# Performance work log

Measured on AMD Instinct MI355X. Metric: run time of the kernel, lower is better.

## Reference

```python
import jax, jax.numpy as jnp
import numpy as np

P_EPS = 1e-6            # nn.PairwiseDistance default eps
ALPHA = 0.25
STD_TARGET = 1.0
NUM_COMMUNITIES = 512   # C = number of unique community ids
BIG = 1e30              # masking value for hard-negative min


def setup_inputs() -> dict:
    key = jax.random.key(0)
    k1, k2, k3 = jax.random.split(key, 3)
    B, N, D, C = 1, 100000, 128, NUM_COMMUNITIES
    node_features = jax.random.normal(k1, (B, N, D), dtype=jnp.float32)
    # row 0: a permutation of node indices; row 1: community of that node.
    perm = jax.random.permutation(k2, N).astype(jnp.int32)
    comm_per_node = jnp.concatenate([
        jnp.arange(C, dtype=jnp.int32),  # guarantee every community appears
        jax.random.randint(k3, (N - C,), 0, C, dtype=jnp.int32),
    ])
    community_belong_list = jnp.stack([perm, comm_per_node[perm]])  # [2, N]
    return {"node_features": node_features, "community_belong_list": community_belong_list}


def reference(node_features, community_belong_list):
    B, N, D = node_features.shape
    C = NUM_COMMUNITIES
    dt = node_features.dtype

    # ---- _community_inverse_permute: invert row-0 permutation, reorder columns ----
    perm = community_belong_list[0]
    inv = jnp.zeros((N,), perm.dtype).at[perm].add(jnp.arange(N, dtype=perm.dtype))
    cbl = community_belong_list[:, inv]          # row0 == arange(N) after this
    comm = cbl[1]                                # [N] community id per node
    src = node_features[:, cbl[0], :]            # [B,N,D] gather (identity order)

    # ---- groupby sum / count -> community means ----
    comm_sum = jnp.zeros((B, C, D), dt).at[:, comm, :].add(src)        # [B,C,D]
    counts = jnp.zeros((C,), dt).at[comm].add(jnp.asarray(1.0, dt))   # [C]
    comm_mean = comm_sum / counts[None, :, None]                      # [B,C,D]

    # ---- cdist(node_features, comm_mean, p=2) -> [B,N,C] ----
    x2 = jnp.sum(node_features * node_features, -1)                   # [B,N]
    c2 = jnp.sum(comm_mean * comm_mean, -1)                           # [B,C]
    dots = jnp.einsum('bnd,bcd->bnc', node_features, comm_mean)
    distance = jnp.sqrt(jnp.maximum(x2[:, :, None] + c2[:, None, :] - 2.0 * dots, 0.0))

    # ---- leave-one-out community mean per node, positive distance ----
    cnt_pn = counts[comm]                                             # [N]
    cnt_m1 = jnp.maximum(cnt_pn - 1.0, 1.0)                           # [N]
    x_minus = jnp.where((cnt_pn == 1.0)[None, :, None], jnp.asarray(0.0, dt), src)
    loo_mean = (comm_sum[:, comm, :] - x_minus) / cnt_m1[None, :, None]
    pos_dist = jnp.sqrt(jnp.sum((loo_mean - src + P_EPS) ** 2, -1))   # [B,N]

    # ---- negatives: all communities except the node's own ----
    own = distance[:, jnp.arange(N), comm]                            # [B,N]
    mean_neg = (jnp.sum(distance, -1) - own) / (C - 1)                # [B,N]
    pos_mask = jnp.zeros((N, C), bool).at[jnp.arange(N), comm].set(True)
    hard_neg = jnp.min(jnp.where(pos_mask[None], jnp.asarray(BIG, dt), distance), -1)

    trip_mean = jnp.maximum(pos_dist - mean_neg + ALPHA, 0.0)
    trip_min = jnp.maximum(pos_dist - hard_neg + ALPHA, 0.0)

    # ---- groupby std (unbiased) per community per feature ----
    sq = jnp.zeros((B, C, D), dt).at[:, comm, :].add((src - comm_mean[:, comm, :]) ** 2)
    std = jnp.sqrt(sq / jnp.maximum(counts - 1.0, 1.0)[None, :, None])

    return (trip_mean.mean(), trip_min.mean(), ((std - STD_TARGET) ** 2).mean())
```

## Files before the change

### kernel.cpp

```cpp
#include <hip/hip_runtime.h>

#define NCOMM 512
#define DIM   128
#define ALPHA 0.25f
#define PEPS  1e-6f
#define BIGF  1e30f
#define TILE_C 16
#define NT    (NCOMM / TILE_C)

typedef __attribute__((ext_vector_type(8))) _Float16 f16x8;
typedef __attribute__((ext_vector_type(4))) float f32x4;

#define GLOAD_LDS16(g, l) __builtin_amdgcn_global_load_lds( \
    (const __attribute__((address_space(1))) void*)(g), \
    (__attribute__((address_space(3))) void*)(l), 16, 0, 0)


__global__ void k_inv(const int* __restrict__ cbl, int* __restrict__ inv, int N) {
    int i = blockIdx.x * 256 + threadIdx.x;
    if (i < N) inv[cbl[i]] = i;
}

__global__ void k_comm(const int* __restrict__ cbl, const int* __restrict__ inv,
                       int* __restrict__ comm, int* __restrict__ idx0,
                       int* __restrict__ counts, int N) {
    __shared__ int h[NCOMM];
    int t = threadIdx.x;
    h[t] = 0; h[t + 256] = 0;
    __syncthreads();
    int j = blockIdx.x * 256 + t;
    if (j < N) {
        int ij = inv[j];
        int c  = cbl[N + ij];
        comm[j] = c;
        idx0[j] = cbl[ij];
        atomicAdd(&h[c], 1);
    }
    __syncthreads();
    int v = h[t];        if (v) atomicAdd(&counts[t], v);
    v = h[t + 256];      if (v) atomicAdd(&counts[t + 256], v);
}

__global__ void k_scan(const int* __restrict__ counts, int* __restrict__ offsets,
                       int* __restrict__ cursor, float* __restrict__ countf) {
    __shared__ int sc[NCOMM];
    int t = threadIdx.x;
    int v0 = counts[t];
    sc[t] = v0;
    __syncthreads();
    for (int off = 1; off < NCOMM; off <<= 1) {
        int v = (t >= off) ? sc[t - off] : 0;
        __syncthreads();
        sc[t] += v;
        __syncthreads();
    }
    int excl = sc[t] - v0;
    offsets[t] = excl;
    cursor[t]  = excl;
    countf[t]  = (float)v0;
}

__global__ void k_sort(const int* __restrict__ comm, int* __restrict__ cursor,
                       int* __restrict__ sorted, int N) {
    __shared__ int h[NCOMM], hb[NCOMM];
    int t = threadIdx.x;
    h[t] = 0; h[t + 256] = 0;
    __syncthreads();
    int j0 = blockIdx.x * 1024 + t;
    int cs[4];
    #pragma unroll
    for (int q = 0; q < 4; ++q) {
        int j = j0 + q * 256;
        cs[q] = (j < N) ? comm[j] : -1;
        if (cs[q] >= 0) atomicAdd(&h[cs[q]], 1);
    }
    __syncthreads();
    int v = h[t];        if (v) hb[t] = atomicAdd(&cursor[t], v);
    v = h[t + 256];      if (v) hb[t + 256] = atomicAdd(&cursor[t + 256], v);
    __syncthreads();
    #pragma unroll
    for (int q = 0; q < 4; ++q) {
        int j = j0 + q * 256;
        if (cs[q] >= 0) {
            int p = atomicAdd(&hb[cs[q]], 1);
            sorted[p] = j;
        }
    }
}


__global__ void __launch_bounds__(256) k_stats(
        const float* __restrict__ NF, const int* __restrict__ idx0,
        const int* __restrict__ sorted, const int* __restrict__ offsets,
        const int* __restrict__ counts,
        float* __restrict__ comm_sum,
        _Float16* __restrict__ CMh, _Float16* __restrict__ CMl,
        float* __restrict__ c2, float* __restrict__ accum) {
    __shared__ int ridx[512];
    __shared__ float4 bufS[256], bufQ[256];
    int c = blockIdx.x, t = threadIdx.x;
    int d4 = t & 31, r = t >> 5;
    int cnt = counts[c], base = offsets[c];
    const float4* NF4 = (const float4*)NF;

    float4 s4 = make_float4(0.f, 0.f, 0.f, 0.f);
    float4 q4 = make_float4(0.f, 0.f, 0.f, 0.f);
    for (int chunk = 0; chunk < cnt; chunk += 512) {
        int m = min(cnt - chunk, 512);
        for (int i = t; i < m; i += 256) ridx[i] = idx0[sorted[base + chunk + i]];
        __syncthreads();
        for (int i = r; i < m; i += 8) {
            float4 v = NF4[(size_t)ridx[i] * 32 + d4];
            s4.x += v.x; s4.y += v.y; s4.z += v.z; s4.w += v.w;
            q4.x = fmaf(v.x, v.x, q4.x); q4.y = fmaf(v.y, v.y, q4.y);
            q4.z = fmaf(v.z, v.z, q4.z); q4.w = fmaf(v.w, v.w, q4.w);
        }
        __syncthreads();
    }
    bufS[t] = s4; bufQ[t] = q4;
    __syncthreads();
    if (t < 128) {
        float4 a = bufS[t], b = bufS[t + 128];
        a.x += b.x; a.y += b.y; a.z += b.z; a.w += b.w; bufS[t] = a;
        float4 e = bufQ[t], f = bufQ[t + 128];
        e.x += f.x; e.y += f.y; e.z += f.z; e.w += f.w; bufQ[t] = e;
    }
    __syncthreads();
    if (t < 64) {
        float4 a = bufS[t], b = bufS[t + 64];
        a.x += b.x; a.y += b.y; a.z += b.z; a.w += b.w; bufS[t] = a;
        float4 e = bufQ[t], f = bufQ[t + 64];
        e.x += f.x; e.y += f.y; e.z += f.z; e.w += f.w; bufQ[t] = e;
    }
    __syncthreads();
    if (t < 32) {
        float4 a = bufS[t], b = bufS[t + 32];
        a.x += b.x; a.y += b.y; a.z += b.z; a.w += b.w;
        float4 e = bufQ[t], f = bufQ[t + 32];
        e.x += f.x; e.y += f.y; e.z += f.z; e.w += f.w;
        float sarr[4] = {a.x, a.y, a.z, a.w};
        float qarr[4] = {e.x, e.y, e.z, e.w};
        float cf = (float)cnt;
        float mm = 0.f, ee = 0.f;
        #pragma unroll
        for (int k = 0; k < 4; ++k) {
            int d = t * 4 + k;
            float s = sarr[k];
            comm_sum[c * DIM + d] = s;
            float m = (cnt > 0) ? s / cf : 0.f;
            _Float16 mh = (_Float16)m;
            CMh[c * DIM + d] = mh;
            CMl[c * DIM + d] = (_Float16)(m - (float)mh);
            float varn = fmaxf(fmaf(-cf * m, m, qarr[k]), 0.f);
            float stdv = sqrtf(varn / fmaxf(cf - 1.f, 1.f));
            float er = stdv - 1.f;
            mm = fmaf(m, m, mm);
            ee = fmaf(er, er, ee);
        }
        #pragma unroll
        for (int msk = 1; msk < 32; msk <<= 1) {
            mm += __shfl_xor(mm, msk);
            ee += __shfl_xor(ee, msk);
        }
        if (t == 0) {
            c2[c] = mm;
            atomicAdd(&accum[2], ee);
        }
    }
}


__global__ void __launch_bounds__(256, 2) k_main(
        const float* __restrict__ NF,
        const _Float16* __restrict__ CMh,
        const _Float16* __restrict__ CMl,
        const float* __restrict__ comm_sum,
        const float* __restrict__ c2g,
        const float* __restrict__ countf,
        const int* __restrict__ comm,
        const int* __restrict__ idx0,
        float* __restrict__ accum, int N) {
    __shared__ _Float16 Bst[4][2][2][TILE_C * DIM];
    __shared__ float c2s[NCOMM];
    __shared__ int   comms[256];
    __shared__ float x2s[256];
    __shared__ float sums[256], mins[256];
    __shared__ float red[8];

    int tid = threadIdx.x;
    int w  = tid >> 6;
    int l  = tid & 63;
    int lr = l & 15;
    int lk = l >> 4;
    int n0 = blockIdx.x * 256;

    int goff[4];
    #pragma unroll
    for (int i = 0; i < 4; ++i) {
        int p = i * 64 + l;
        int row = p >> 4, cp = p & 15;
        goff[i] = (row * 16 + (cp ^ row)) * 8;
    }
    auto stage = [&](int tt, int b) {
        int base = tt * (TILE_C * DIM);
        _Float16* lh = &Bst[w][b][0][0];
        _Float16* ll = &Bst[w][b][1][0];
        #pragma unroll
        for (int i = 0; i < 4; ++i) {
            GLOAD_LDS16(CMh + base + goff[i], lh + i * 512);
            GLOAD_LDS16(CMl + base + goff[i], ll + i * 512);
        }
    };
    stage(0, 0);

    c2s[tid]       = c2g[tid];
    c2s[tid + 256] = c2g[tid + 256];
    {
        int gn = n0 + tid;
        comms[tid] = (gn < N) ? comm[gn] : -1;
    }

    f16x8 ah[4][4];
    #pragma unroll
    for (int mf = 0; mf < 4; ++mf) {
        int n = n0 + w * 64 + mf * 16 + lr;
        const float4* src = (const float4*)NF + (size_t)n * 32 + lk * 2;
        float p2 = 0.f;
        #pragma unroll
        for (int ks = 0; ks < 4; ++ks) {
            float4 v0 = make_float4(0.f, 0.f, 0.f, 0.f), v1 = v0;
            if (n < N) { v0 = src[ks * 8]; v1 = src[ks * 8 + 1]; }
            float fr[8] = {v0.x, v0.y, v0.z, v0.w, v1.x, v1.y, v1.z, v1.w};
            f16x8 hh;
            #pragma unroll
            for (int t = 0; t < 8; ++t) {
                hh[t] = (_Float16)fr[t];
                p2 = fmaf(fr[t], fr[t], p2);
            }
            ah[mf][ks] = hh;
        }
        p2 += __shfl_xor(p2, 16);
        p2 += __shfl_xor(p2, 32);
        if (lk == 0) x2s[w * 64 + mf * 16 + lr] = -0.5f * p2;
    }
    __syncthreads();

    int cnv[4][4];
    float sumv[4][4], minv[4][4];
    #pragma unroll
    for (int mf = 0; mf < 4; ++mf)
        #pragma unroll
        for (int j = 0; j < 4; ++j) {
            cnv[mf][j] = comms[w * 64 + mf * 16 + lk * 4 + j];
            sumv[mf][j] = 0.f; minv[mf][j] = BIGF;
        }

    int buf = 0;
    for (int tt = 0; tt < NT; ++tt) {
        if (tt + 1 < NT) {
            stage(tt + 1, buf ^ 1);
            asm volatile("s_waitcnt vmcnt(8)" ::: "memory");
        } else {
            asm volatile("s_waitcnt vmcnt(0)" ::: "memory");
        }
        __builtin_amdgcn_sched_barrier(0);

        const _Float16* bhp = &Bst[w][buf][0][0];
        const _Float16* blp = &Bst[w][buf][1][0];
        f16x8 bh[4], bl[4];
        #pragma unroll
        for (int ks = 0; ks < 4; ++ks) {
            int ch = (ks * 4 + lk) ^ lr;
            bh[ks] = *(const f16x8*)&bhp[(size_t)(lr * 16 + ch) * 8];
            bl[ks] = *(const f16x8*)&blp[(size_t)(lr * 16 + ch) * 8];
        }
        f32x4 acc[4];
        #pragma unroll
        for (int mf = 0; mf < 4; ++mf)
            acc[mf] = *(const f32x4*)&x2s[w * 64 + mf * 16 + lk * 4];

        #pragma unroll
        for (int ks = 0; ks < 4; ++ks) {
            #pragma unroll
            for (int mf = 0; mf < 4; ++mf)
                acc[mf] = __builtin_amdgcn_mfma_f32_16x16x32_f16(ah[mf][ks], bh[ks], acc[mf], 0, 0, 0);
            #pragma unroll
            for (int mf = 0; mf < 4; ++mf)
                acc[mf] = __builtin_amdgcn_mfma_f32_16x16x32_f16(ah[mf][ks], bl[ks], acc[mf], 0, 0, 0);
        }

        int ccol = tt * TILE_C + lr;
        float c2v = c2s[ccol];
        #pragma unroll
        for (int mf = 0; mf < 4; ++mf)
            #pragma unroll
            for (int j = 0; j < 4; ++j) {
                float d2 = fmaf(-2.f, acc[mf][j], c2v);
                float da = __builtin_amdgcn_sqrtf(fmaxf(d2, 0.f));
                sumv[mf][j] += da;
                minv[mf][j] = fminf(minv[mf][j], (cnv[mf][j] == ccol) ? BIGF : da);
            }
        buf ^= 1;
    }

    #pragma unroll
    for (int mf = 0; mf < 4; ++mf)
        #pragma unroll
        for (int j = 0; j < 4; ++j) {
            float sv = sumv[mf][j], mv = minv[mf][j];
            #pragma unroll
            for (int msk = 1; msk < 16; msk <<= 1) {
                sv += __shfl_xor(sv, msk);
                mv = fminf(mv, __shfl_xor(mv, msk));
            }
            if (lr == 0) {
                int idx = w * 64 + mf * 16 + lk * 4 + j;
                sums[idx] = sv; mins[idx] = mv;
            }
        }
    __syncthreads();

    float tmean = 0.f, tminv = 0.f;
    {
        int ln = tid;
        int n = n0 + ln;
        if (n < N) {
            int cnode = comms[ln];
            float cf  = countf[cnode];
            float cm1 = fmaxf(cf - 1.f, 1.f);
            float rs  = 1.f / cm1;
            bool single = (cf == 1.f);
            const float4* srow = (const float4*)(NF + (size_t)idx0[n] * DIM);
            const float4* csum = (const float4*)(comm_sum + (size_t)cnode * DIM);
            float q = 0.f, dot = 0.f;
            #pragma unroll 8
            for (int m = 0; m < 32; ++m) {
                float4 sv = srow[m];
                float4 cs = csum[m];
                float4 xm = single ? make_float4(0.f, 0.f, 0.f, 0.f) : sv;
                float lx = (cs.x - xm.x) * rs - sv.x + PEPS;
                float ly = (cs.y - xm.y) * rs - sv.y + PEPS;
                float lz = (cs.z - xm.z) * rs - sv.z + PEPS;
                float lw = (cs.w - xm.w) * rs - sv.w + PEPS;
                q = fmaf(lx, lx, fmaf(ly, ly, fmaf(lz, lz, fmaf(lw, lw, q))));
                dot = fmaf(sv.x, cs.x, fmaf(sv.y, cs.y, fmaf(sv.z, cs.z, fmaf(sv.w, cs.w, dot))));
            }
            float pos = sqrtf(q);
            float x2 = -2.f * x2s[ln];
            float ownd2 = x2 + c2s[cnode] - 2.f * (dot / cf);
            float own = sqrtf(fmaxf(ownd2, 0.f));
            float mean_neg = (sums[ln] - own) * (1.f / (float)(NCOMM - 1));
            tmean = fmaxf(pos - mean_neg + ALPHA, 0.f);
            tminv = fmaxf(pos - mins[ln] + ALPHA, 0.f);
        }
    }
    #pragma unroll
    for (int msk = 1; msk < 64; msk <<= 1) {
        tmean += __shfl_xor(tmean, msk);
        tminv += __shfl_xor(tminv, msk);
    }
    if ((tid & 63) == 0) { red[w * 2] = tmean; red[w * 2 + 1] = tminv; }
    __syncthreads();
    if (tid == 0) {
        atomicAdd(&accum[0], red[0] + red[2] + red[4] + red[6]);
        atomicAdd(&accum[1], red[1] + red[3] + red[5] + red[7]);
    }
}

__global__ void k_final(const float* __restrict__ accum, float* __restrict__ out, int N) {
    if (threadIdx.x == 0) {
        out[0] = accum[0] / (float)N;
        out[1] = accum[1] / (float)N;
        out[2] = accum[2] / (float)(NCOMM * DIM);
    }
}


extern "C" void kernel_launch(void* const* d_in, const int* in_sizes, int n_in,
                              void* d_out, int out_size, void* d_ws, size_t ws_size,
                              hipStream_t stream) {
    const float* NF  = (const float*)d_in[0];
    const int*   CBL = (const int*)d_in[1];
    int N = in_sizes[1] / 2;
    if (N <= 0) return;

    char* ws = (char*)d_ws;
    float* accum   = (float*)ws;
    int*   counts  = (int*)(ws + 16);
    int*   cursor  = (int*)(ws + 16 + 2048);
    int*   offsets = (int*)(ws + 16 + 2 * 2048);
    float* countf  = (float*)(ws + 16 + 3 * 2048);
    float* c2      = (float*)(ws + 16 + 4 * 2048);
    char* p = ws + 16 + 5 * 2048;
    int* inv    = (int*)p; p += (size_t)N * 4;
    int* comm   = (int*)p; p += (size_t)N * 4;
    int* idx0   = (int*)p; p += (size_t)N * 4;
    int* sorted = (int*)p; p += (size_t)N * 4;
    float* comm_sum = (float*)p; p += (size_t)NCOMM * DIM * 4;
    _Float16* CMh = (_Float16*)p; p += (size_t)NCOMM * DIM * 2;
    _Float16* CMl = (_Float16*)p;

    hipMemsetAsync(d_ws, 0, 16 + 2048, stream);

    int nb = (N + 255) / 256;
    k_inv <<<nb, 256, 0, stream>>>(CBL, inv, N);
    k_comm<<<nb, 256, 0, stream>>>(CBL, inv, comm, idx0, counts, N);
    k_scan<<<1, NCOMM, 0, stream>>>(counts, offsets, cursor, countf);
    int nb4 = (N + 1023) / 1024;
    k_sort<<<nb4, 256, 0, stream>>>(comm, cursor, sorted, N);
    k_stats<<<NCOMM, 256, 0, stream>>>(NF, idx0, sorted, offsets, counts,
                                       comm_sum, CMh, CMl, c2, accum);
    int mb = (N + 255) / 256;
    k_main<<<mb, 256, 0, stream>>>(NF, CMh, CMl, comm_sum, c2, countf,
                                   comm, idx0, accum, N);
    k_final<<<1, 64, 0, stream>>>(accum, (float*)d_out, N);
}
```

Baseline: 129.9 us.

## Fuse permutation prep, drop idx0 indirection, share centroid tiles block-wide

Replaces the inverse-permutation and community kernels with a single scatter kernel, since the gathered row index equals the node index. Removes the idx0 indirection from the stats and main kernels. In the main kernel, centroid tiles are staged once per block with 32-wide tiles instead of per wave. The x2 term is hoisted out of the loop and occupancy is raised to 3 blocks per SM. This trades per-wave async waits for block barriers, which adds synchronisation but cuts LDS use and redundant global traffic.

```diff
diff --git a/kernel.cpp b/kernel.cpp
--- a/kernel.cpp
+++ b/kernel.cpp
@@ -5,7 +5,7 @@
 #define ALPHA 0.25f
 #define PEPS  1e-6f
 #define BIGF  1e30f
-#define TILE_C 16
+#define TILE_C 32
 #define NT    (NCOMM / TILE_C)
 
 typedef __attribute__((ext_vector_type(8))) _Float16 f16x8;
@@ -16,24 +16,17 @@
     (__attribute__((address_space(3))) void*)(l), 16, 0, 0)
 
 
-__global__ void k_inv(const int* __restrict__ cbl, int* __restrict__ inv, int N) {
-    int i = blockIdx.x * 256 + threadIdx.x;
-    if (i < N) inv[cbl[i]] = i;
-}
-
-__global__ void k_comm(const int* __restrict__ cbl, const int* __restrict__ inv,
-                       int* __restrict__ comm, int* __restrict__ idx0,
+__global__ void k_prep(const int* __restrict__ cbl, int* __restrict__ comm,
                        int* __restrict__ counts, int N) {
     __shared__ int h[NCOMM];
     int t = threadIdx.x;
     h[t] = 0; h[t + 256] = 0;
     __syncthreads();
-    int j = blockIdx.x * 256 + t;
-    if (j < N) {
-        int ij = inv[j];
-        int c  = cbl[N + ij];
-        comm[j] = c;
-        idx0[j] = cbl[ij];
+    int i = blockIdx.x * 256 + t;
+    if (i < N) {
+        int p = cbl[i];
+        int c = cbl[N + i];
+        comm[p] = c;
         atomicAdd(&h[c], 1);
     }
     __syncthreads();
@@ -90,7 +83,7 @@
 
 
 __global__ void __launch_bounds__(256) k_stats(
-        const float* __restrict__ NF, const int* __restrict__ idx0,
+        const float* __restrict__ NF,
         const int* __restrict__ sorted, const int* __restrict__ offsets,
         const int* __restrict__ counts,
         float* __restrict__ comm_sum,
@@ -107,7 +100,7 @@
     float4 q4 = make_float4(0.f, 0.f, 0.f, 0.f);
     for (int chunk = 0; chunk < cnt; chunk += 512) {
         int m = min(cnt - chunk, 512);
-        for (int i = t; i < m; i += 256) ridx[i] = idx0[sorted[base + chunk + i]];
+        for (int i = t; i < m; i += 256) ridx[i] = sorted[base + chunk + i];
         __syncthreads();
         for (int i = r; i < m; i += 8) {
             float4 v = NF4[(size_t)ridx[i] * 32 + d4];
@@ -170,7 +163,7 @@
 }
 
 
-__global__ void __launch_bounds__(256, 2) k_main(
+__global__ void __launch_bounds__(256, 3) k_main(
         const float* __restrict__ NF,
         const _Float16* __restrict__ CMh,
         const _Float16* __restrict__ CMl,
@@ -178,12 +171,11 @@
         const float* __restrict__ c2g,
         const float* __restrict__ countf,
         const int* __restrict__ comm,
-        const int* __restrict__ idx0,
         float* __restrict__ accum, int N) {
-    __shared__ _Float16 Bst[4][2][2][TILE_C * DIM];
+    __shared__ _Float16 Bst[2][2][TILE_C * DIM];
     __shared__ float c2s[NCOMM];
     __shared__ int   comms[256];
-    __shared__ float x2s[256];
+    __shared__ float x2sh[256];
     __shared__ float sums[256], mins[256];
     __shared__ float red[8];
 
@@ -194,21 +186,17 @@
     int lk = l >> 4;
     int n0 = blockIdx.x * 256;
 
-    int goff[4];
-    #pragma unroll
-    for (int i = 0; i < 4; ++i) {
-        int p = i * 64 + l;
-        int row = p >> 4, cp = p & 15;
-        goff[i] = (row * 16 + (cp ^ row)) * 8;
-    }
     auto stage = [&](int tt, int b) {
-        int base = tt * (TILE_C * DIM);
-        _Float16* lh = &Bst[w][b][0][0];
-        _Float16* ll = &Bst[w][b][1][0];
-        #pragma unroll
-        for (int i = 0; i < 4; ++i) {
-            GLOAD_LDS16(CMh + base + goff[i], lh + i * 512);
-            GLOAD_LDS16(CMl + base + goff[i], ll + i * 512);
+        int c0 = tt * TILE_C;
+        #pragma unroll
+        for (int rnd = 0; rnd < 2; ++rnd) {
+            int p = rnd * 256 + tid;
+            int row = p >> 4, cp = p & 15;
+            size_t g = ((size_t)(c0 + row) * 16 + (cp ^ (row & 15))) * 8;
+            _Float16* dh = &Bst[b][0][(size_t)(rnd * 256 + w * 64) * 8];
+            _Float16* dl = &Bst[b][1][(size_t)(rnd * 256 + w * 64) * 8];
+            GLOAD_LDS16(CMh + g, dh);
+            GLOAD_LDS16(CMl + g, dl);
         }
     };
     stage(0, 0);
@@ -241,65 +229,64 @@
         }
         p2 += __shfl_xor(p2, 16);
         p2 += __shfl_xor(p2, 32);
-        if (lk == 0) x2s[w * 64 + mf * 16 + lr] = -0.5f * p2;
-    }
-    __syncthreads();
-
+        if (lk == 0) x2sh[w * 64 + mf * 16 + lr] = -0.5f * p2;
+    }
+    __syncthreads();
+
+    f32x4 x2v[4];
     int cnv[4][4];
     float sumv[4][4], minv[4][4];
     #pragma unroll
-    for (int mf = 0; mf < 4; ++mf)
+    for (int mf = 0; mf < 4; ++mf) {
+        x2v[mf] = *(const f32x4*)&x2sh[w * 64 + mf * 16 + lk * 4];
         #pragma unroll
         for (int j = 0; j < 4; ++j) {
             cnv[mf][j] = comms[w * 64 + mf * 16 + lk * 4 + j];
             sumv[mf][j] = 0.f; minv[mf][j] = BIGF;
         }
+    }
 
     int buf = 0;
     for (int tt = 0; tt < NT; ++tt) {
-        if (tt + 1 < NT) {
-            stage(tt + 1, buf ^ 1);
-            asm volatile("s_waitcnt vmcnt(8)" ::: "memory");
-        } else {
-            asm volatile("s_waitcnt vmcnt(0)" ::: "memory");
-        }
-        __builtin_amdgcn_sched_barrier(0);
-
-        const _Float16* bhp = &Bst[w][buf][0][0];
-        const _Float16* blp = &Bst[w][buf][1][0];
-        f16x8 bh[4], bl[4];
-        #pragma unroll
-        for (int ks = 0; ks < 4; ++ks) {
-            int ch = (ks * 4 + lk) ^ lr;
-            bh[ks] = *(const f16x8*)&bhp[(size_t)(lr * 16 + ch) * 8];
-            bl[ks] = *(const f16x8*)&blp[(size_t)(lr * 16 + ch) * 8];
-        }
-        f32x4 acc[4];
-        #pragma unroll
-        for (int mf = 0; mf < 4; ++mf)
-            acc[mf] = *(const f32x4*)&x2s[w * 64 + mf * 16 + lk * 4];
-
-        #pragma unroll
-        for (int ks = 0; ks < 4; ++ks) {
+        if (tt + 1 < NT) stage(tt + 1, buf ^ 1);
+
+        #pragma unroll
+        for (int s = 0; s < 2; ++s) {
+            int rbase = s * 16 + lr;
+            const _Float16* bhp = &Bst[buf][0][0];
+            const _Float16* blp = &Bst[buf][1][0];
+            f16x8 bh[4], bl[4];
+            #pragma unroll
+            for (int ks = 0; ks < 4; ++ks) {
+                int ch = (ks * 4 + lk) ^ lr;
+                bh[ks] = *(const f16x8*)&bhp[(size_t)(rbase * 16 + ch) * 8];
+                bl[ks] = *(const f16x8*)&blp[(size_t)(rbase * 16 + ch) * 8];
+            }
+            f32x4 acc[4];
+            #pragma unroll
+            for (int mf = 0; mf < 4; ++mf) acc[mf] = x2v[mf];
+            #pragma unroll
+            for (int ks = 0; ks < 4; ++ks) {
+                #pragma unroll
+                for (int mf = 0; mf < 4; ++mf)
+                    acc[mf] = __builtin_amdgcn_mfma_f32_16x16x32_f16(ah[mf][ks], bh[ks], acc[mf], 0, 0, 0);
+                #pragma unroll
+                for (int mf = 0; mf < 4; ++mf)
+                    acc[mf] = __builtin_amdgcn_mfma_f32_16x16x32_f16(ah[mf][ks], bl[ks], acc[mf], 0, 0, 0);
+            }
+            int ccol = tt * TILE_C + s * 16 + lr;
+            float c2v = c2s[ccol];
             #pragma unroll
             for (int mf = 0; mf < 4; ++mf)
-                acc[mf] = __builtin_amdgcn_mfma_f32_16x16x32_f16(ah[mf][ks], bh[ks], acc[mf], 0, 0, 0);
-            #pragma unroll
-            for (int mf = 0; mf < 4; ++mf)
-                acc[mf] = __builtin_amdgcn_mfma_f32_16x16x32_f16(ah[mf][ks], bl[ks], acc[mf], 0, 0, 0);
-        }
-
-        int ccol = tt * TILE_C + lr;
-        float c2v = c2s[ccol];
-        #pragma unroll
-        for (int mf = 0; mf < 4; ++mf)
-            #pragma unroll
-            for (int j = 0; j < 4; ++j) {
-                float d2 = fmaf(-2.f, acc[mf][j], c2v);
-                float da = __builtin_amdgcn_sqrtf(fmaxf(d2, 0.f));
-                sumv[mf][j] += da;
-                minv[mf][j] = fminf(minv[mf][j], (cnv[mf][j] == ccol) ? BIGF : da);
-            }
+                #pragma unroll
+                for (int j = 0; j < 4; ++j) {
+                    float d2 = fmaf(-2.f, acc[mf][j], c2v);
+                    float da = __builtin_amdgcn_sqrtf(fmaxf(d2, 0.f));
+                    sumv[mf][j] += da;
+                    minv[mf][j] = fminf(minv[mf][j], (cnv[mf][j] == ccol) ? BIGF : da);
+                }
+        }
+        __syncthreads();
         buf ^= 1;
     }
 
@@ -330,7 +317,7 @@
             float cm1 = fmaxf(cf - 1.f, 1.f);
             float rs  = 1.f / cm1;
             bool single = (cf == 1.f);
-            const float4* srow = (const float4*)(NF + (size_t)idx0[n] * DIM);
+            const float4* srow = (const float4*)NF + (size_t)n * 32;
             const float4* csum = (const float4*)(comm_sum + (size_t)cnode * DIM);
             float q = 0.f, dot = 0.f;
             #pragma unroll 8
@@ -346,7 +333,7 @@
                 dot = fmaf(sv.x, cs.x, fmaf(sv.y, cs.y, fmaf(sv.z, cs.z, fmaf(sv.w, cs.w, dot))));
             }
             float pos = sqrtf(q);
-            float x2 = -2.f * x2s[ln];
+            float x2 = -2.f * x2sh[ln];
             float ownd2 = x2 + c2s[cnode] - 2.f * (dot / cf);
             float own = sqrtf(fmaxf(ownd2, 0.f));
             float mean_neg = (sums[ln] - own) * (1.f / (float)(NCOMM - 1));
@@ -392,9 +379,7 @@
     float* countf  = (float*)(ws + 16 + 3 * 2048);
     float* c2      = (float*)(ws + 16 + 4 * 2048);
     char* p = ws + 16 + 5 * 2048;
-    int* inv    = (int*)p; p += (size_t)N * 4;
     int* comm   = (int*)p; p += (size_t)N * 4;
-    int* idx0   = (int*)p; p += (size_t)N * 4;
     int* sorted = (int*)p; p += (size_t)N * 4;
     float* comm_sum = (float*)p; p += (size_t)NCOMM * DIM * 4;
     _Float16* CMh = (_Float16*)p; p += (size_t)NCOMM * DIM * 2;
@@ -403,15 +388,14 @@
     hipMemsetAsync(d_ws, 0, 16 + 2048, stream);
 
     int nb = (N + 255) / 256;
-    k_inv <<<nb, 256, 0, stream>>>(CBL, inv, N);
-    k_comm<<<nb, 256, 0, stream>>>(CBL, inv, comm, idx0, counts, N);
+    k_prep<<<nb, 256, 0, stream>>>(CBL, comm, counts, N);
     k_scan<<<1, NCOMM, 0, stream>>>(counts, offsets, cursor, countf);
     int nb4 = (N + 1023) / 1024;
     k_sort<<<nb4, 256, 0, stream>>>(comm, cursor, sorted, N);
-    k_stats<<<NCOMM, 256, 0, stream>>>(NF, idx0, sorted, offsets, counts,
+    k_stats<<<NCOMM, 256, 0, stream>>>(NF, sorted, offsets, counts,
                                        comm_sum, CMh, CMl, c2, accum);
     int mb = (N + 255) / 256;
     k_main<<<mb, 256, 0, stream>>>(NF, CMh, CMl, comm_sum, c2, countf,
-                                   comm, idx0, accum, N);
+                                   comm, accum, N);
     k_final<<<1, 64, 0, stream>>>(accum, (float*)d_out, N);
 }
```

Measured after the change: 132.2 us. Within noise of the previous version (+1.8%).
